# Optimization experiments

Measured on AMD Instinct MI355X. Metric: run time of the kernel, lower is better.

The kernel has to match this reference:

```python
import jax, jax.numpy as jnp
import numpy as np

TAU = 2.0
TIMESTEP = 24
WAIT = 12
START = 0
LOG_BASE = 1.0 / np.log(TAU)                       # 1/ln(tau)
V_TH0 = TAU ** (TIMESTEP - 1) / LOG_BASE / 2.0     # initial firing threshold


def setup_inputs() -> dict:
    key = jax.random.key(0)
    T = START + TIMESTEP + WAIT                    # 36 sequential calls
    x = jax.random.normal(key, (T, 32, 64, 1024), dtype=jnp.float32)
    return {"x": x}


def reference(x):
    """Unrolls the stateful per-timestep WTA_layer_Neuron.forward over the
    time axis of x with lax.scan. Neuron model (WTA_neuron, v_reset=None):
    integrate-and-fire with soft reset and an exponentially decaying
    threshold (th /= tau each firing step), charging-only during the wait
    phase -- the standard semantics for this temporal-coded WTA conversion.
    Returns the spike train [T, B, H, N] (the per-call return value x)."""
    T, B, H, N = x.shape
    dt = x.dtype
    v0 = jnp.zeros((B, H, N), dt)
    block0 = jnp.zeros((B, H, N), dt)
    blk_in0 = jnp.ones((B, H), dt)                 # torch.ones_like(x.max(-1).values)
    ss0 = jnp.zeros((B, H), dt)
    th0 = jnp.asarray(V_TH0, dt)
    ss_scale = jnp.asarray(1.0 / TAU ** (TIMESTEP - 1), dt)

    def step(carry, xt):
        v, th, block, block_input, spike_sum, t = carry
        # input-side WTA masking
        tp_max = xt.max(-1)                                    # [B, H]
        xt = xt - tp_max[..., None] * block_input[..., None]
        block_input = jnp.where(tp_max > 0.0, jnp.zeros_like(block_input), block_input)
        # IF neuron: charge always, fire only after the wait phase
        v = v + xt
        fire = t >= START + WAIT
        spike = jnp.where(fire & (v >= th), jnp.ones_like(v), jnp.zeros_like(v))
        v = v - spike * th                                      # soft reset (v_reset=None)
        th = jnp.where(fire, th / TAU, th)                      # threshold decay
        # output-side WTA blocking: each neuron spikes at most once
        out = jnp.where(block == 1, jnp.zeros_like(spike), spike)
        block = jnp.where(out > 0, jnp.ones_like(block), block)
        # spike_sum *= tau; spike_sum += out.sum(-1) / tau**(T-1)
        spike_sum = jnp.where(fire, spike_sum * TAU + out.sum(-1) * ss_scale, spike_sum)
        return (v, th, block, block_input, spike_sum, t + 1), out

    init = (v0, th0, block0, blk_in0, ss0, jnp.int32(0))
    _, spikes = jax.lax.scan(step, init, x)
    return spikes
```

## Files before the change

kernel.cpp:

```cpp
#include <hip/hip_runtime.h>


constexpr int T_TOTAL = 36;
constexpr int T_FIRE0 = 12;
constexpr int NPAIR   = 32 * 64;
constexpr int NN      = 1024;

using f32x4 = __attribute__((ext_vector_type(4))) float;

__device__ __forceinline__ void load4(f32x4 (&xa)[4], const float* __restrict__ xt, int lane) {
#pragma unroll
    for (int k = 0; k < 4; ++k)
        xa[k] = __builtin_nontemporal_load((const f32x4*)(xt + 4 * lane + 256 * k));
}

template <bool FIRE>
__device__ __forceinline__ void process_step(const f32x4 (&xa)[4], float (&v)[16],
                                             unsigned& blockmask, float& bi, float& th,
                                             float* __restrict__ ot, int lane) {
    float m = xa[0][0];
#pragma unroll
    for (int k = 0; k < 4; ++k)
        m = fmaxf(m, fmaxf(fmaxf(xa[k][0], xa[k][1]), fmaxf(xa[k][2], xa[k][3])));
#pragma unroll
    for (int off = 32; off >= 1; off >>= 1)
        m = fmaxf(m, __shfl_xor(m, off, 64));

    const float sub = m * bi;
    if (!FIRE) {
#pragma unroll
        for (int k = 0; k < 4; ++k) {
#pragma unroll
            for (int j = 0; j < 4; ++j)
                v[4 * k + j] += xa[k][j] - sub;
        }
        const f32x4 z = {0.f, 0.f, 0.f, 0.f};
#pragma unroll
        for (int k = 0; k < 4; ++k)
            __builtin_nontemporal_store(z, (f32x4*)(ot + 4 * lane + 256 * k));
    } else {
#pragma unroll
        for (int k = 0; k < 4; ++k) {
            f32x4 ov;
#pragma unroll
            for (int j = 0; j < 4; ++j) {
                const int idx = 4 * k + j;
                float vn = v[idx] + (xa[k][j] - sub);
                const bool spike = (vn >= th);
                v[idx] = spike ? (vn - th) : vn;
                const bool blocked = (blockmask >> idx) & 1u;
                ov[j] = (spike && !blocked) ? 1.0f : 0.0f;
                if (spike) blockmask |= (1u << idx);
            }
            __builtin_nontemporal_store(ov, (f32x4*)(ot + 4 * lane + 256 * k));
        }
        th *= 0.5f;
    }
    if (m > 0.0f) bi = 0.0f;
}

__global__ __launch_bounds__(256) void wta_kernel(const float* __restrict__ x,
                                                  float* __restrict__ out) {
    const int gtid = blockIdx.x * 256 + threadIdx.x;
    const int pair = gtid >> 6;
    const int lane = threadIdx.x & 63;
    const size_t pair_off = (size_t)pair * NN;

    float v[16];
#pragma unroll
    for (int i = 0; i < 16; ++i) v[i] = 0.0f;
    unsigned blockmask = 0;
    float bi = 1.0f;

    const double ln2 = 0.6931471805599453;
    float th = (float)(8388608.0 / (1.0 / ln2) / 2.0);

    const float* xb = x + pair_off;
    float* ob = out + pair_off;
    const size_t stride = (size_t)NPAIR * NN;

    f32x4 A[4], B[4];
    load4(A, xb, lane);

    for (int t = 0; t < T_FIRE0; t += 2) {
        load4(B, xb + (size_t)(t + 1) * stride, lane);
        process_step<false>(A, v, blockmask, bi, th, ob + (size_t)t * stride, lane);
        load4(A, xb + (size_t)(t + 2) * stride, lane);
        process_step<false>(B, v, blockmask, bi, th, ob + (size_t)(t + 1) * stride, lane);
    }

    for (int t = T_FIRE0; t < T_TOTAL - 2; t += 2) {
        load4(B, xb + (size_t)(t + 1) * stride, lane);
        process_step<true>(A, v, blockmask, bi, th, ob + (size_t)t * stride, lane);
        load4(A, xb + (size_t)(t + 2) * stride, lane);
        process_step<true>(B, v, blockmask, bi, th, ob + (size_t)(t + 1) * stride, lane);
    }
    {
        const int t = T_TOTAL - 2;
        load4(B, xb + (size_t)(t + 1) * stride, lane);
        process_step<true>(A, v, blockmask, bi, th, ob + (size_t)t * stride, lane);
        process_step<true>(B, v, blockmask, bi, th, ob + (size_t)(t + 1) * stride, lane);
    }
}

extern "C" void kernel_launch(void* const* d_in, const int* in_sizes, int n_in,
                              void* d_out, int out_size, void* d_ws, size_t ws_size,
                              hipStream_t stream) {
    const float* x = (const float*)d_in[0];
    float* out = (float*)d_out;
    wta_kernel<<<dim3(NPAIR / 4), dim3(256), 0, stream>>>(x, out);
}
```

Before: 102.8 us.

## Split each row across a 256-thread block with shared-memory max reduction

Each (B,H) row of 1024 neurons was handled by one wavefront holding 16 values per lane. Now a full 256-thread block covers one row with 4 values per thread, and a per-step cross-wave max goes through double-buffered shared memory with a __syncthreads. The aim is to raise the number of resident waves and outstanding loads to better hide memory latency on this streaming kernel. The cost is a block barrier every timestep and less data in flight per thread.

Result: slower. 109.9 us (+6.9%).

```diff
diff --git a/kernel.cpp b/kernel.cpp
--- a/kernel.cpp
+++ b/kernel.cpp
@@ -8,98 +8,92 @@
 
 using f32x4 = __attribute__((ext_vector_type(4))) float;
 
-__device__ __forceinline__ void load4(f32x4 (&xa)[4], const float* __restrict__ xt, int lane) {
-#pragma unroll
-    for (int k = 0; k < 4; ++k)
-        xa[k] = __builtin_nontemporal_load((const f32x4*)(xt + 4 * lane + 256 * k));
-}
-
 template <bool FIRE>
-__device__ __forceinline__ void process_step(const f32x4 (&xa)[4], float (&v)[16],
+__device__ __forceinline__ void process_step(const f32x4 xa, float (&v)[4],
                                              unsigned& blockmask, float& bi, float& th,
-                                             float* __restrict__ ot, int lane) {
-    float m = xa[0][0];
-#pragma unroll
-    for (int k = 0; k < 4; ++k)
-        m = fmaxf(m, fmaxf(fmaxf(xa[k][0], xa[k][1]), fmaxf(xa[k][2], xa[k][3])));
+                                             float* __restrict__ ot, int wid, int lane,
+                                             int par, float (*smax)[4]) {
+    float mw = fmaxf(fmaxf(xa[0], xa[1]), fmaxf(xa[2], xa[3]));
 #pragma unroll
     for (int off = 32; off >= 1; off >>= 1)
-        m = fmaxf(m, __shfl_xor(m, off, 64));
+        mw = fmaxf(mw, __shfl_xor(mw, off, 64));
+    if (lane == 0) smax[par][wid] = mw;
+    __syncthreads();
+    const float m = fmaxf(fmaxf(smax[par][0], smax[par][1]),
+                          fmaxf(smax[par][2], smax[par][3]));
 
     const float sub = m * bi;
     if (!FIRE) {
 #pragma unroll
-        for (int k = 0; k < 4; ++k) {
+        for (int j = 0; j < 4; ++j)
+            v[j] += xa[j] - sub;
+        const f32x4 z = {0.f, 0.f, 0.f, 0.f};
+        __builtin_nontemporal_store(z, (f32x4*)ot);
+    } else {
+        f32x4 ov;
 #pragma unroll
-            for (int j = 0; j < 4; ++j)
-                v[4 * k + j] += xa[k][j] - sub;
+        for (int j = 0; j < 4; ++j) {
+            float vn = v[j] + (xa[j] - sub);
+            const bool spike = (vn >= th);
+            v[j] = spike ? (vn - th) : vn;
+            const bool blocked = (blockmask >> j) & 1u;
+            ov[j] = (spike && !blocked) ? 1.0f : 0.0f;
+            if (spike) blockmask |= (1u << j);
         }
-        const f32x4 z = {0.f, 0.f, 0.f, 0.f};
-#pragma unroll
-        for (int k = 0; k < 4; ++k)
-            __builtin_nontemporal_store(z, (f32x4*)(ot + 4 * lane + 256 * k));
-    } else {
-#pragma unroll
-        for (int k = 0; k < 4; ++k) {
-            f32x4 ov;
-#pragma unroll
-            for (int j = 0; j < 4; ++j) {
-                const int idx = 4 * k + j;
-                float vn = v[idx] + (xa[k][j] - sub);
-                const bool spike = (vn >= th);
-                v[idx] = spike ? (vn - th) : vn;
-                const bool blocked = (blockmask >> idx) & 1u;
-                ov[j] = (spike && !blocked) ? 1.0f : 0.0f;
-                if (spike) blockmask |= (1u << idx);
-            }
-            __builtin_nontemporal_store(ov, (f32x4*)(ot + 4 * lane + 256 * k));
-        }
+        __builtin_nontemporal_store(ov, (f32x4*)ot);
         th *= 0.5f;
     }
     if (m > 0.0f) bi = 0.0f;
 }
 
-__global__ __launch_bounds__(256) void wta_kernel(const float* __restrict__ x,
-                                                  float* __restrict__ out) {
-    const int gtid = blockIdx.x * 256 + threadIdx.x;
-    const int pair = gtid >> 6;
-    const int lane = threadIdx.x & 63;
-    const size_t pair_off = (size_t)pair * NN;
+__global__ __launch_bounds__(256, 8) void wta_kernel(const float* __restrict__ x,
+                                                     float* __restrict__ out) {
+    const int pair = blockIdx.x;
+    const int tid  = threadIdx.x;
+    const int wid  = tid >> 6;
+    const int lane = tid & 63;
+    const size_t base = (size_t)pair * NN + 4 * (size_t)tid;
+    const size_t stride = (size_t)NPAIR * NN;
 
-    float v[16];
-#pragma unroll
-    for (int i = 0; i < 16; ++i) v[i] = 0.0f;
+    __shared__ float smax[2][4];
+
+    float v[4] = {0.f, 0.f, 0.f, 0.f};
     unsigned blockmask = 0;
     float bi = 1.0f;
 
     const double ln2 = 0.6931471805599453;
     float th = (float)(8388608.0 / (1.0 / ln2) / 2.0);
 
-    const float* xb = x + pair_off;
-    float* ob = out + pair_off;
-    const size_t stride = (size_t)NPAIR * NN;
+    const float* xp = x + base;
+    float* op = out + base;
 
-    f32x4 A[4], B[4];
-    load4(A, xb, lane);
+    f32x4 A = __builtin_nontemporal_load((const f32x4*)(xp));
+    f32x4 B;
 
     for (int t = 0; t < T_FIRE0; t += 2) {
-        load4(B, xb + (size_t)(t + 1) * stride, lane);
-        process_step<false>(A, v, blockmask, bi, th, ob + (size_t)t * stride, lane);
-        load4(A, xb + (size_t)(t + 2) * stride, lane);
-        process_step<false>(B, v, blockmask, bi, th, ob + (size_t)(t + 1) * stride, lane);
+        B = __builtin_nontemporal_load((const f32x4*)(xp + (size_t)(t + 1) * stride));
+        process_step<false>(A, v, blockmask, bi, th, op + (size_t)t * stride,
+                            wid, lane, t & 1, smax);
+        A = __builtin_nontemporal_load((const f32x4*)(xp + (size_t)(t + 2) * stride));
+        process_step<false>(B, v, blockmask, bi, th, op + (size_t)(t + 1) * stride,
+                            wid, lane, (t + 1) & 1, smax);
     }
 
     for (int t = T_FIRE0; t < T_TOTAL - 2; t += 2) {
-        load4(B, xb + (size_t)(t + 1) * stride, lane);
-        process_step<true>(A, v, blockmask, bi, th, ob + (size_t)t * stride, lane);
-        load4(A, xb + (size_t)(t + 2) * stride, lane);
-        process_step<true>(B, v, blockmask, bi, th, ob + (size_t)(t + 1) * stride, lane);
+        B = __builtin_nontemporal_load((const f32x4*)(xp + (size_t)(t + 1) * stride));
+        process_step<true>(A, v, blockmask, bi, th, op + (size_t)t * stride,
+                           wid, lane, t & 1, smax);
+        A = __builtin_nontemporal_load((const f32x4*)(xp + (size_t)(t + 2) * stride));
+        process_step<true>(B, v, blockmask, bi, th, op + (size_t)(t + 1) * stride,
+                           wid, lane, (t + 1) & 1, smax);
     }
     {
         const int t = T_TOTAL - 2;
-        load4(B, xb + (size_t)(t + 1) * stride, lane);
-        process_step<true>(A, v, blockmask, bi, th, ob + (size_t)t * stride, lane);
-        process_step<true>(B, v, blockmask, bi, th, ob + (size_t)(t + 1) * stride, lane);
+        B = __builtin_nontemporal_load((const f32x4*)(xp + (size_t)(t + 1) * stride));
+        process_step<true>(A, v, blockmask, bi, th, op + (size_t)t * stride,
+                           wid, lane, t & 1, smax);
+        process_step<true>(B, v, blockmask, bi, th, op + (size_t)(t + 1) * stride,
+                           wid, lane, (t + 1) & 1, smax);
     }
 }
 
@@ -108,5 +102,5 @@
                               hipStream_t stream) {
     const float* x = (const float*)d_in[0];
     float* out = (float*)d_out;
-    wta_kernel<<<dim3(NPAIR / 4), dim3(256), 0, stream>>>(x, out);
+    wta_kernel<<<dim3(NPAIR), dim3(256), 0, stream>>>(x, out);
 }
```
